# Kernel optimization log

Hardware: AMD Instinct MI355X
Metric: run time of the kernel (lower is better)

Reference implementation:

```python
import jax, jax.numpy as jnp
import numpy as np

TEMPERATURE = 0.07
MASK_VAL = -9e15
EPS = 1e-8

def setup_inputs() -> dict:
    key = jax.random.key(0)
    features = jax.random.normal(key, (8192, 256), dtype=jnp.float32)
    return {"features": features}

def reference(features):
    # features: [N, D]
    N = features.shape[0]
    norm = jnp.linalg.norm(features, axis=-1, keepdims=True)
    f = features / jnp.maximum(norm, EPS)
    # cosine similarity via GEMM: [N, N]
    sim = f @ f.T
    idx = jnp.arange(N)
    # mask self-similarity BEFORE temperature scaling (as in the torch code)
    sim = jnp.where(idx[:, None] == idx[None, :], MASK_VAL, sim)
    sim = sim / TEMPERATURE
    # positive of row i is column (i - N//2) mod N (eye rolled by N//2 along dim 0)
    pos_col = (idx - N // 2) % N
    pos = sim[idx, pos_col]
    nll = -pos + jax.nn.logsumexp(sim, axis=-1)
    return nll.mean()
```

## Files before the change

### kernel.cpp

```cpp
#include <hip/hip_runtime.h>
#include <hip/hip_bf16.h>
#include <math.h>

#define N_ROWS 8192
#define D_DIM  256
#define HALF_N 4096
#define NBLK   640u
#define INV_T      14.285714285714286f
#define SCALE_LOG2 20.609929155556620f
#define NEG_SCALE  -20.609929155556620f
#define EPSV   1e-8f

typedef __attribute__((ext_vector_type(8))) short bf16x8;
typedef __attribute__((ext_vector_type(4))) float f32x4;

#define AS1 __attribute__((address_space(1)))
#define AS3 __attribute__((address_space(3)))
#define AGT __HIP_MEMORY_SCOPE_AGENT

__device__ unsigned g_done = 0;

__device__ inline unsigned short f2bf(float x) {
    unsigned int u = __float_as_uint(x);
    unsigned int r = (u + 0x7fffu + ((u >> 16) & 1u)) >> 16;
    return (unsigned short)r;
}

__global__ __launch_bounds__(256) void k_prep(const float* __restrict__ feat,
                                              unsigned short* __restrict__ fbf,
                                              float* __restrict__ sumexp,
                                              float* __restrict__ posv) {
    const int tid = threadIdx.x, w = tid >> 6, lane = tid & 63;
    const int row = blockIdx.x * 4 + w;
    const int pc  = (row + HALF_N) & (N_ROWS - 1);

    const float4 v = ((const float4*)(feat + row * D_DIM))[lane];
    const float4 c = ((const float4*)(feat + pc  * D_DIM))[lane];
    float ss  = v.x*v.x + v.y*v.y + v.z*v.z + v.w*v.w;
    float dab = v.x*c.x + v.y*c.y + v.z*c.z + v.w*c.w;
    float dbb = c.x*c.x + c.y*c.y + c.z*c.z + c.w*c.w;
    #pragma unroll
    for (int off = 32; off; off >>= 1) {
        ss  += __shfl_xor(ss,  off);
        dab += __shfl_xor(dab, off);
        dbb += __shfl_xor(dbb, off);
    }
    const float na = fmaxf(sqrtf(ss), EPSV);
    const float sc = 1.f / na;
    ushort4 o;
    o.x = f2bf(v.x * sc); o.y = f2bf(v.y * sc);
    o.z = f2bf(v.z * sc); o.w = f2bf(v.w * sc);
    ((ushort4*)(fbf + row * D_DIM))[lane] = o;
    if (lane == 0)
        posv[row] = INV_T - (dab / (na * fmaxf(sqrtf(dbb), EPSV))) * INV_T;
    if (tid < 4) sumexp[blockIdx.x * 4 + tid] = 0.f;
}

__global__ __launch_bounds__(256, 2) void k_simfin(const unsigned short* __restrict__ fbf,
                                                   float* __restrict__ sumexp,
                                                   const float* __restrict__ posv,
                                                   float* __restrict__ out) {
    __shared__ __align__(16) char Bs[16384];
    __shared__ float red[4];
    __shared__ int lastBlk;
    const int tid  = threadIdx.x;
    const int lane = tid & 63;
    const int w    = tid >> 6;
    const int q    = lane >> 4, l15 = lane & 15;
    const int b    = blockIdx.x;

    int tt, jtBegin, jtEnd;
    if (b < 512) { tt = b;                      jtBegin = 0;            jtEnd = 8; }
    else         { tt = 512 + ((b - 512) >> 3); jtBegin = (b - 512) & 7; jtEnd = jtBegin + 1; }

    int rt = (int)((sqrtf(8.f * (float)tt + 1.f) - 1.f) * 0.5f);
    while ((rt + 1) * (rt + 2) / 2 <= tt) ++rt;
    while (rt * (rt + 1) / 2 > tt) --rt;
    const int cs = tt - rt * (rt + 1) / 2;
    const bool isDiag = (rt == cs);
    const int rowBase = rt * 256 + w * 64;

#define STAGE(colRow0) do {                                                   \
        const char* Bg_ = (const char*)fbf + (size_t)(colRow0) * 512;         \
        _Pragma("unroll")                                                     \
        for (int i_ = 0; i_ < 4; ++i_) {                                      \
            const int idx_ = i_ * 256 + tid;                                  \
            const int col_ = idx_ >> 5;                                       \
            const int cir_ = idx_ & 31;                                       \
            __builtin_amdgcn_global_load_lds(                                 \
                (const AS1 void*)(Bg_ + col_ * 512 + ((cir_ ^ (col_ & 7)) << 4)), \
                (AS3 void*)(Bs + idx_ * 16), 16, 0, 0);                       \
        }                                                                     \
    } while (0)

    bf16x8 afrag[8][4];
    #pragma unroll
    for (int t = 0; t < 8; ++t)
        #pragma unroll
        for (int ri = 0; ri < 4; ++ri)
            afrag[t][ri] = *(const bf16x8*)(fbf + (rowBase + ri*16 + l15) * D_DIM
                                                + t*32 + q*8);

    float rsum[4][4];
    #pragma unroll
    for (int ri = 0; ri < 4; ++ri)
        #pragma unroll
        for (int r = 0; r < 4; ++r) rsum[ri][r] = 0.f;

    STAGE(cs * 256 + jtBegin * 32);

    for (int jt = jtBegin; jt < jtEnd; ++jt) {
        const int colBase = cs * 256 + jt * 32;

        __syncthreads();

        f32x4 acc[4][2];
        #pragma unroll
        for (int ri = 0; ri < 4; ++ri)
            #pragma unroll
            for (int ci = 0; ci < 2; ++ci) acc[ri][ci] = (f32x4){0.f, 0.f, 0.f, 0.f};

        #pragma unroll
        for (int t = 0; t < 8; ++t) {
            bf16x8 bfrag[2];
            #pragma unroll
            for (int ci = 0; ci < 2; ++ci) {
                const int c   = ci * 16 + l15;
                const int cir = t * 4 + q;
                bfrag[ci] = *(const bf16x8*)(Bs + c * 512 + ((cir ^ (c & 7)) << 4));
            }
            #pragma unroll
            for (int ri = 0; ri < 4; ++ri)
                #pragma unroll
                for (int ci = 0; ci < 2; ++ci)
                    acc[ri][ci] = __builtin_amdgcn_mfma_f32_16x16x32_bf16(
                        afrag[t][ri], bfrag[ci], acc[ri][ci], 0, 0, 0);
        }

        if (jt + 1 < jtEnd) {
            __syncthreads();
            STAGE(cs * 256 + (jt + 1) * 32);
        }

        if (isDiag) {
            #pragma unroll
            for (int ri = 0; ri < 4; ++ri) {
                const int trow = rowBase + ri * 16;
                #pragma unroll
                for (int ci = 0; ci < 2; ++ci) {
                    const int tcol = colBase + ci * 16;
                    if (trow == tcol) {
                        #pragma unroll
                        for (int r = 0; r < 4; ++r) {
                            const float e = __builtin_amdgcn_exp2f(
                                __builtin_fmaf(acc[ri][ci][r], SCALE_LOG2, NEG_SCALE));
                            rsum[ri][r] += (q * 4 + r == l15) ? 0.f : e;
                        }
                    } else {
                        #pragma unroll
                        for (int r = 0; r < 4; ++r)
                            rsum[ri][r] += __builtin_amdgcn_exp2f(
                                __builtin_fmaf(acc[ri][ci][r], SCALE_LOG2, NEG_SCALE));
                    }
                }
            }
        } else {
            float csum0 = 0.f, csum1 = 0.f;
            #pragma unroll
            for (int ri = 0; ri < 4; ++ri) {
                #pragma unroll
                for (int r = 0; r < 4; ++r) {
                    const float e0 = __builtin_amdgcn_exp2f(
                        __builtin_fmaf(acc[ri][0][r], SCALE_LOG2, NEG_SCALE));
                    const float e1 = __builtin_amdgcn_exp2f(
                        __builtin_fmaf(acc[ri][1][r], SCALE_LOG2, NEG_SCALE));
                    rsum[ri][r] += e0 + e1;
                    csum0 += e0;
                    csum1 += e1;
                }
            }
            csum0 += __shfl_xor(csum0, 16); csum0 += __shfl_xor(csum0, 32);
            csum1 += __shfl_xor(csum1, 16); csum1 += __shfl_xor(csum1, 32);
            if (q == 0)      atomicAdd(&sumexp[colBase      + l15], csum0);
            else if (q == 1) atomicAdd(&sumexp[colBase + 16 + l15], csum1);
        }
    }

    #pragma unroll
    for (int ri = 0; ri < 4; ++ri)
        #pragma unroll
        for (int r = 0; r < 4; ++r) {
            float s = rsum[ri][r];
            s += __shfl_xor(s, 1);
            s += __shfl_xor(s, 2);
            s += __shfl_xor(s, 4);
            s += __shfl_xor(s, 8);
            if (l15 == 0)
                atomicAdd(&sumexp[rowBase + ri * 16 + q * 4 + r], s);
        }
#undef STAGE

    __syncthreads();
    if (tid == 0) {
        const unsigned old = __hip_atomic_fetch_add(&g_done, 1u, __ATOMIC_ACQ_REL, AGT);
        lastBlk = ((old % NBLK) == NBLK - 1u);
    }
    __syncthreads();
    if (lastBlk) {
        float wsum = 0.f;
        for (int i = tid; i < N_ROWS; i += 256)
            wsum += posv[i] + logf(sumexp[i]);
        #pragma unroll
        for (int off = 32; off; off >>= 1) wsum += __shfl_xor(wsum, off);
        if (lane == 0) red[w] = wsum;
        __syncthreads();
        if (tid == 0)
            out[0] = (red[0] + red[1] + red[2] + red[3]) * (1.f / N_ROWS);
    }
}

extern "C" void kernel_launch(void* const* d_in, const int* in_sizes, int n_in,
                              void* d_out, int out_size, void* d_ws, size_t ws_size,
                              hipStream_t stream) {
    const float* feat = (const float*)d_in[0];
    char* ws = (char*)d_ws;
    unsigned short* fbf = (unsigned short*)ws;
    float* sumexp = (float*)(ws + 4u * 1024u * 1024u);
    float* posv   = (float*)(ws + 4u * 1024u * 1024u + 32768u);

    k_prep  <<<N_ROWS / 4, 256, 0, stream>>>(feat, fbf, sumexp, posv);
    k_simfin<<<NBLK,       256, 0, stream>>>(fbf, sumexp, posv, (float*)d_out);
}
```

Measured before the change: 115.3 us.

## Split fused tile kernel into tiles, strips and finalize launches

Splits the single kernel that ran both full 256x256 tiles and the split last-row-strip blocks into two kernels, k_tiles (512 blocks) and k_strips (128 blocks), and moves the final log-sum reduction into a separate single-block k_fin launch. This removes the global atomic done-counter and the last-block check, and lets each kernel specialise its control flow (the tile loop now has a fixed trip count with unroll 1). The cost is two extra kernel launches and their serialization on the stream, and the strip blocks can no longer overlap with the tile blocks.

```diff
diff --git a/kernel.cpp b/kernel.cpp
--- a/kernel.cpp
+++ b/kernel.cpp
@@ -5,7 +5,6 @@
 #define N_ROWS 8192
 #define D_DIM  256
 #define HALF_N 4096
-#define NBLK   640u
 #define INV_T      14.285714285714286f
 #define SCALE_LOG2 20.609929155556620f
 #define NEG_SCALE  -20.609929155556620f
@@ -16,15 +15,69 @@
 
 #define AS1 __attribute__((address_space(1)))
 #define AS3 __attribute__((address_space(3)))
-#define AGT __HIP_MEMORY_SCOPE_AGENT
-
-__device__ unsigned g_done = 0;
 
 __device__ inline unsigned short f2bf(float x) {
     unsigned int u = __float_as_uint(x);
     unsigned int r = (u + 0x7fffu + ((u >> 16) & 1u)) >> 16;
     return (unsigned short)r;
 }
+
+#define STAGE_DEF(colRow0) do {                                               \
+        const char* Bg_ = (const char*)fbf + (size_t)(colRow0) * 512;         \
+        _Pragma("unroll")                                                     \
+        for (int i_ = 0; i_ < 4; ++i_) {                                      \
+            const int idx_ = i_ * 256 + tid;                                  \
+            const int col_ = idx_ >> 5;                                       \
+            const int cir_ = idx_ & 31;                                       \
+            __builtin_amdgcn_global_load_lds(                                 \
+                (const AS1 void*)(Bg_ + col_ * 512 + ((cir_ ^ (col_ & 7)) << 4)), \
+                (AS3 void*)(Bs + idx_ * 16), 16, 0, 0);                       \
+        }                                                                     \
+    } while (0)
+
+#define LOAD_A_DEF(rowBase_) do {                                             \
+        _Pragma("unroll")                                                     \
+        for (int t_ = 0; t_ < 8; ++t_)                                        \
+            _Pragma("unroll")                                                 \
+            for (int ri_ = 0; ri_ < 4; ++ri_)                                 \
+                afrag[t_][ri_] = *(const bf16x8*)(fbf                         \
+                    + ((rowBase_) + ri_*16 + l15) * D_DIM + t_*32 + q*8);     \
+    } while (0)
+
+#define MFMA_STRIP_DEF() do {                                                 \
+        _Pragma("unroll")                                                     \
+        for (int t_ = 0; t_ < 8; ++t_) {                                      \
+            bf16x8 bfrag[2];                                                  \
+            _Pragma("unroll")                                                 \
+            for (int ci_ = 0; ci_ < 2; ++ci_) {                               \
+                const int c_   = ci_ * 16 + l15;                              \
+                const int cir_ = t_ * 4 + q;                                  \
+                bfrag[ci_] = *(const bf16x8*)(Bs + c_ * 512                   \
+                                              + ((cir_ ^ (c_ & 7)) << 4));    \
+            }                                                                 \
+            _Pragma("unroll")                                                 \
+            for (int ri_ = 0; ri_ < 4; ++ri_)                                 \
+                _Pragma("unroll")                                             \
+                for (int ci_ = 0; ci_ < 2; ++ci_)                             \
+                    acc[ri_][ci_] = __builtin_amdgcn_mfma_f32_16x16x32_bf16(  \
+                        afrag[t_][ri_], bfrag[ci_], acc[ri_][ci_], 0, 0, 0);  \
+        }                                                                     \
+    } while (0)
+
+#define FLUSH_RSUM_DEF(rowBase_) do {                                         \
+        _Pragma("unroll")                                                     \
+        for (int ri_ = 0; ri_ < 4; ++ri_)                                     \
+            _Pragma("unroll")                                                 \
+            for (int r_ = 0; r_ < 4; ++r_) {                                  \
+                float s_ = rsum[ri_][r_];                                     \
+                s_ += __shfl_xor(s_, 1);                                      \
+                s_ += __shfl_xor(s_, 2);                                      \
+                s_ += __shfl_xor(s_, 4);                                      \
+                s_ += __shfl_xor(s_, 8);                                      \
+                if (l15 == 0)                                                 \
+                    atomicAdd(&sumexp[(rowBase_) + ri_ * 16 + q * 4 + r_], s_); \
+            }                                                                 \
+    } while (0)
 
 __global__ __launch_bounds__(256) void k_prep(const float* __restrict__ feat,
                                               unsigned short* __restrict__ fbf,
@@ -56,23 +109,15 @@
     if (tid < 4) sumexp[blockIdx.x * 4 + tid] = 0.f;
 }
 
-__global__ __launch_bounds__(256, 2) void k_simfin(const unsigned short* __restrict__ fbf,
-                                                   float* __restrict__ sumexp,
-                                                   const float* __restrict__ posv,
-                                                   float* __restrict__ out) {
+__global__ __launch_bounds__(256, 2) void k_tiles(const unsigned short* __restrict__ fbf,
+                                                  float* __restrict__ sumexp) {
     __shared__ __align__(16) char Bs[16384];
-    __shared__ float red[4];
-    __shared__ int lastBlk;
     const int tid  = threadIdx.x;
     const int lane = tid & 63;
     const int w    = tid >> 6;
     const int q    = lane >> 4, l15 = lane & 15;
-    const int b    = blockIdx.x;
-
-    int tt, jtBegin, jtEnd;
-    if (b < 512) { tt = b;                      jtBegin = 0;            jtEnd = 8; }
-    else         { tt = 512 + ((b - 512) >> 3); jtBegin = (b - 512) & 7; jtEnd = jtBegin + 1; }
-
+
+    const int tt = blockIdx.x;
     int rt = (int)((sqrtf(8.f * (float)tt + 1.f) - 1.f) * 0.5f);
     while ((rt + 1) * (rt + 2) / 2 <= tt) ++rt;
     while (rt * (rt + 1) / 2 > tt) --rt;
@@ -80,66 +125,34 @@
     const bool isDiag = (rt == cs);
     const int rowBase = rt * 256 + w * 64;
 
-#define STAGE(colRow0) do {                                                   \
-        const char* Bg_ = (const char*)fbf + (size_t)(colRow0) * 512;         \
-        _Pragma("unroll")                                                     \
-        for (int i_ = 0; i_ < 4; ++i_) {                                      \
-            const int idx_ = i_ * 256 + tid;                                  \
-            const int col_ = idx_ >> 5;                                       \
-            const int cir_ = idx_ & 31;                                       \
-            __builtin_amdgcn_global_load_lds(                                 \
-                (const AS1 void*)(Bg_ + col_ * 512 + ((cir_ ^ (col_ & 7)) << 4)), \
-                (AS3 void*)(Bs + idx_ * 16), 16, 0, 0);                       \
-        }                                                                     \
-    } while (0)
+    STAGE_DEF(cs * 256);
 
     bf16x8 afrag[8][4];
-    #pragma unroll
-    for (int t = 0; t < 8; ++t)
+    LOAD_A_DEF(rowBase);
+
+    float rsum[4][4];
+    #pragma unroll
+    for (int ri = 0; ri < 4; ++ri)
+        #pragma unroll
+        for (int r = 0; r < 4; ++r) rsum[ri][r] = 0.f;
+
+    #pragma unroll 1
+    for (int jt = 0; jt < 8; ++jt) {
+        const int colBase = cs * 256 + jt * 32;
+
+        __syncthreads();
+
+        f32x4 acc[4][2];
         #pragma unroll
         for (int ri = 0; ri < 4; ++ri)
-            afrag[t][ri] = *(const bf16x8*)(fbf + (rowBase + ri*16 + l15) * D_DIM
-                                                + t*32 + q*8);
-
-    float rsum[4][4];
-    #pragma unroll
-    for (int ri = 0; ri < 4; ++ri)
-        #pragma unroll
-        for (int r = 0; r < 4; ++r) rsum[ri][r] = 0.f;
-
-    STAGE(cs * 256 + jtBegin * 32);
-
-    for (int jt = jtBegin; jt < jtEnd; ++jt) {
-        const int colBase = cs * 256 + jt * 32;
-
-        __syncthreads();
-
-        f32x4 acc[4][2];
-        #pragma unroll
-        for (int ri = 0; ri < 4; ++ri)
             #pragma unroll
             for (int ci = 0; ci < 2; ++ci) acc[ri][ci] = (f32x4){0.f, 0.f, 0.f, 0.f};
 
-        #pragma unroll
-        for (int t = 0; t < 8; ++t) {
-            bf16x8 bfrag[2];
-            #pragma unroll
-            for (int ci = 0; ci < 2; ++ci) {
-                const int c   = ci * 16 + l15;
-                const int cir = t * 4 + q;
-                bfrag[ci] = *(const bf16x8*)(Bs + c * 512 + ((cir ^ (c & 7)) << 4));
-            }
-            #pragma unroll
-            for (int ri = 0; ri < 4; ++ri)
-                #pragma unroll
-                for (int ci = 0; ci < 2; ++ci)
-                    acc[ri][ci] = __builtin_amdgcn_mfma_f32_16x16x32_bf16(
-                        afrag[t][ri], bfrag[ci], acc[ri][ci], 0, 0, 0);
-        }
-
-        if (jt + 1 < jtEnd) {
+        MFMA_STRIP_DEF();
+
+        if (jt < 7) {
             __syncthreads();
-            STAGE(cs * 256 + (jt + 1) * 32);
+            STAGE_DEF(cs * 256 + (jt + 1) * 32);
         }
 
         if (isDiag) {
@@ -186,37 +199,105 @@
         }
     }
 
+    FLUSH_RSUM_DEF(rowBase);
+}
+
+__global__ __launch_bounds__(256, 2) void k_strips(const unsigned short* __restrict__ fbf,
+                                                   float* __restrict__ sumexp) {
+    __shared__ __align__(16) char Bs[16384];
+    const int tid  = threadIdx.x;
+    const int lane = tid & 63;
+    const int w    = tid >> 6;
+    const int q    = lane >> 4, l15 = lane & 15;
+
+    const int b  = blockIdx.x;
+    const int cs = 16 + (b >> 3);
+    const int jt = b & 7;
+    const bool isDiag = (cs == 31);
+    const int rowBase = 31 * 256 + w * 64;
+    const int colBase = cs * 256 + jt * 32;
+
+    STAGE_DEF(colBase);
+
+    bf16x8 afrag[8][4];
+    LOAD_A_DEF(rowBase);
+
+    float rsum[4][4];
     #pragma unroll
     for (int ri = 0; ri < 4; ++ri)
         #pragma unroll
-        for (int r = 0; r < 4; ++r) {
-            float s = rsum[ri][r];
-            s += __shfl_xor(s, 1);
-            s += __shfl_xor(s, 2);
-            s += __shfl_xor(s, 4);
-            s += __shfl_xor(s, 8);
-            if (l15 == 0)
-                atomicAdd(&sumexp[rowBase + ri * 16 + q * 4 + r], s);
+        for (int r = 0; r < 4; ++r) rsum[ri][r] = 0.f;
+
+    __syncthreads();
+
+    f32x4 acc[4][2];
+    #pragma unroll
+    for (int ri = 0; ri < 4; ++ri)
+        #pragma unroll
+        for (int ci = 0; ci < 2; ++ci) acc[ri][ci] = (f32x4){0.f, 0.f, 0.f, 0.f};
+
+    MFMA_STRIP_DEF();
+
+    if (isDiag) {
+        #pragma unroll
+        for (int ri = 0; ri < 4; ++ri) {
+            const int trow = rowBase + ri * 16;
+            #pragma unroll
+            for (int ci = 0; ci < 2; ++ci) {
+                const int tcol = colBase + ci * 16;
+                if (trow == tcol) {
+                    #pragma unroll
+                    for (int r = 0; r < 4; ++r) {
+                        const float e = __builtin_amdgcn_exp2f(
+                            __builtin_fmaf(acc[ri][ci][r], SCALE_LOG2, NEG_SCALE));
+                        rsum[ri][r] += (q * 4 + r == l15) ? 0.f : e;
+                    }
+                } else {
+                    #pragma unroll
+                    for (int r = 0; r < 4; ++r)
+                        rsum[ri][r] += __builtin_amdgcn_exp2f(
+                            __builtin_fmaf(acc[ri][ci][r], SCALE_LOG2, NEG_SCALE));
+                }
+            }
         }
-#undef STAGE
-
+    } else {
+        float csum0 = 0.f, csum1 = 0.f;
+        #pragma unroll
+        for (int ri = 0; ri < 4; ++ri) {
+            #pragma unroll
+            for (int r = 0; r < 4; ++r) {
+                const float e0 = __builtin_amdgcn_exp2f(
+                    __builtin_fmaf(acc[ri][0][r], SCALE_LOG2, NEG_SCALE));
+                const float e1 = __builtin_amdgcn_exp2f(
+                    __builtin_fmaf(acc[ri][1][r], SCALE_LOG2, NEG_SCALE));
+                rsum[ri][r] += e0 + e1;
+                csum0 += e0;
+                csum1 += e1;
+            }
+        }
+        csum0 += __shfl_xor(csum0, 16); csum0 += __shfl_xor(csum0, 32);
+        csum1 += __shfl_xor(csum1, 16); csum1 += __shfl_xor(csum1, 32);
+        if (q == 0)      atomicAdd(&sumexp[colBase      + l15], csum0);
+        else if (q == 1) atomicAdd(&sumexp[colBase + 16 + l15], csum1);
+    }
+
+    FLUSH_RSUM_DEF(rowBase);
+}
+
+__global__ __launch_bounds__(256) void k_fin(const float* __restrict__ sumexp,
+                                             const float* __restrict__ posv,
+                                             float* __restrict__ out) {
+    __shared__ float red[4];
+    const int tid = threadIdx.x, w = tid >> 6, lane = tid & 63;
+    float wsum = 0.f;
+    for (int i = tid; i < N_ROWS; i += 256)
+        wsum += posv[i] + logf(sumexp[i]);
+    #pragma unroll
+    for (int off = 32; off; off >>= 1) wsum += __shfl_xor(wsum, off);
+    if (lane == 0) red[w] = wsum;
     __syncthreads();
-    if (tid == 0) {
-        const unsigned old = __hip_atomic_fetch_add(&g_done, 1u, __ATOMIC_ACQ_REL, AGT);
-        lastBlk = ((old % NBLK) == NBLK - 1u);
-    }
-    __syncthreads();
-    if (lastBlk) {
-        float wsum = 0.f;
-        for (int i = tid; i < N_ROWS; i += 256)
-            wsum += posv[i] + logf(sumexp[i]);
-        #pragma unroll
-        for (int off = 32; off; off >>= 1) wsum += __shfl_xor(wsum, off);
-        if (lane == 0) red[w] = wsum;
-        __syncthreads();
-        if (tid == 0)
-            out[0] = (red[0] + red[1] + red[2] + red[3]) * (1.f / N_ROWS);
-    }
+    if (tid == 0)
+        out[0] = (red[0] + red[1] + red[2] + red[3]) * (1.f / N_ROWS);
 }
 
 extern "C" void kernel_launch(void* const* d_in, const int* in_sizes, int n_in,
@@ -229,5 +310,7 @@
     float* posv   = (float*)(ws + 4u * 1024u * 1024u + 32768u);
 
     k_prep  <<<N_ROWS / 4, 256, 0, stream>>>(feat, fbf, sumexp, posv);
-    k_simfin<<<NBLK,       256, 0, stream>>>(fbf, sumexp, posv, (float*)d_out);
-}
+    k_tiles <<<512,        256, 0, stream>>>(fbf, sumexp);
+    k_strips<<<128,        256, 0, stream>>>(fbf, sumexp);
+    k_fin   <<<1,          256, 0, stream>>>(sumexp, posv, (float*)d_out);
+}
```

New measurement: 115.8 us. About the same (+0.5%).
